# Optimization experiments

Measured on AMD Instinct MI355X. Metric: run time of the kernel, lower is better.

## Reference

```python
import jax, jax.numpy as jnp
import numpy as np

T, B, H = 512, 64, 1024

def setup_inputs() -> dict:
    key = jax.random.key(0)
    ks = jax.random.split(key, 16)
    names_mat = ['W_ir', 'W_hr', 'W_iz', 'W_hz', 'W_in', 'W_hn']
    names_vec = ['b_ir', 'b_hr', 'b_iz', 'b_hz', 'b_in', 'b_hn']
    inp = {
        'input_': jax.random.normal(ks[0], (T, B, H), dtype=jnp.float32),
        'hidden0': jax.random.normal(ks[1], (B, H), dtype=jnp.float32),
    }
    for i, n in enumerate(names_mat):
        inp[n] = jax.random.normal(ks[2 + i], (H, H), dtype=jnp.float32)
    for i, n in enumerate(names_vec):
        inp[n] = jax.random.normal(ks[8 + i], (H,), dtype=jnp.float32)
    # W = randn(H) * T, b = randn(1) in the original forward; made explicit here
    inp['W_out'] = jax.random.normal(ks[14], (H,), dtype=jnp.float32) * T
    inp['b_out'] = jax.random.normal(ks[15], (1,), dtype=jnp.float32)
    return inp

def reference(input_, hidden0, W_ir, W_hr, W_iz, W_hz, W_in, W_hn,
              b_ir, b_hr, b_iz, b_hz, b_in, b_hn, W_out, b_out):
    h = input_.shape[2]
    # permutation matrix is identity -> lower = tril(ones)
    lower = jnp.tril(jnp.ones((h, h), dtype=input_.dtype))
    Wir, Whr = W_ir * lower, W_hr * lower
    Wiz, Whz = W_iz * lower, W_hz * lower
    Win, Whn = W_in * lower, W_hn * lower

    def step(hid, x):
        # mask == x in the original call: cell(x, lower, x, hidden)
        r = jax.nn.sigmoid(x @ Wir + b_ir * x + hid @ Whr + b_hr)
        z = jax.nn.sigmoid(x @ Wiz + b_iz * x + hid @ Whz + b_hz)
        n = jnp.tanh(x @ Win + b_in * x + r * (hid @ Whn + b_hn))
        hid_new = hid * z + (1.0 - z) * n
        label = jax.nn.sigmoid(hid_new * W_out + b_out) * x  # [B, H]
        return hid_new, label

    _, labels = jax.lax.scan(step, hidden0, input_)  # labels: [T, B, H]
    ans_f = jnp.max(labels, axis=-1)                 # [T, B]
    ans = jnp.where(ans_f >= 0.5, 1, -1).astype(jnp.int32)
    return ans
```

## Files before the change

kernel.cpp:

```cpp
#include <hip/hip_runtime.h>

#define T_DIM 512
#define B_DIM 64
#define H_DIM 1024
#define NBLK 32
#define RING 64
#define AHEAD 62
#define KSLOT 33
#define APITCH 1032
#define FSTR 1024

typedef __attribute__((ext_vector_type(8))) short bf16x8;
typedef __attribute__((ext_vector_type(4))) float f32x4;


__device__ __forceinline__ unsigned short f2bf(float f) {
    unsigned u = __float_as_uint(f);
    unsigned r = (u + 0x7FFFu + ((u >> 16) & 1u)) >> 16;
    return (unsigned short)r;
}
__device__ __forceinline__ unsigned pack2(float a, float b) {
    return (unsigned)f2bf(a) | ((unsigned)f2bf(b) << 16);
}

__global__ __launch_bounds__(128) void prep_pack(
    const float* __restrict__ Wir, const float* __restrict__ Wiz, const float* __restrict__ Win,
    const float* __restrict__ Whr, const float* __restrict__ Whz, const float* __restrict__ Whn,
    unsigned short* __restrict__ Wpk)
{
    const float* srcs[6] = {Wir, Wiz, Win, Whr, Whz, Whn};
    const int bid   = blockIdx.x;
    const int g     = blockIdx.y;
    const int jt    = bid >> 6;
    const int jtile = (bid >> 5) & 1;
    const int ksrel = bid & 31;
    if (ksrel >= NBLK - jt) return;
    const int t    = threadIdx.x;
    const int lane = t >> 1, e0 = (t & 1) * 4;
    const float* src = srcs[g];
    const int j  = 32 * jt + 16 * jtile + (lane & 15);
    const int kb = (jt + ksrel) * 32 + (lane >> 4) * 8 + e0;
    ushort4 o; unsigned short* po = (unsigned short*)&o;
    #pragma unroll
    for (int i = 0; i < 4; ++i) {
        const int k = kb + i;
        const float w = (k >= j) ? src[(size_t)k * H_DIM + j] : 0.0f;
        po[i] = f2bf(w);
    }
    const size_t idx = ((((size_t)(jt * 2 + jtile) * KSLOT + ksrel) * 6 + g) * 64 + lane) * 8 + e0;
    *(ushort4*)(Wpk + idx) = o;
}

__global__ __launch_bounds__(256) void init_h(const float* __restrict__ h0,
                                              unsigned short* __restrict__ hring,
                                              unsigned* __restrict__ prog)
{
    if (blockIdx.x < 256) {
        const int i = blockIdx.x * 256 + threadIdx.x;
        hring[i] = f2bf(h0[i]);
    } else {
        unsigned* p = prog + (size_t)(blockIdx.x - 256) * 8192 + threadIdx.x;
        #pragma unroll
        for (int k = 0; k < 32; ++k) p[k * 256] = 0u;
    }
}

__global__ __launch_bounds__(512) void gru_main(
    const float* __restrict__ x,
    const unsigned short* __restrict__ Wpk,
    const float* __restrict__ bir, const float* __restrict__ bhr,
    const float* __restrict__ biz, const float* __restrict__ bhz,
    const float* __restrict__ bin_, const float* __restrict__ bhn,
    const float* __restrict__ Wout, const float* __restrict__ bout,
    const float* __restrict__ h0,
    unsigned short* __restrict__ hring,
    float* __restrict__ pmax,
    unsigned* __restrict__ prog)
{
    __shared__ __align__(16) unsigned short axf[8 * APITCH];
    __shared__ __align__(16) unsigned short ahf[8 * APITCH];
    __shared__ __align__(16) unsigned short zblk[8];
    __shared__ float red[8][6][64][4];
    __shared__ float hown[8][33];
    __shared__ unsigned short hb[8][32];

    const int tid  = threadIdx.x;
    const int lane = tid & 63;
    const int wv   = tid >> 6;

    const int jt = blockIdx.x & 31;
    const int bg = blockIdx.x >> 5;
    const int b0 = bg * 8;

    const int kcol0 = 32 * jt;
    const int CHN   = (H_DIM - kcol0) >> 3;
    const int cnt   = NBLK - jt;
    const int jtile = wv >> 2;
    const int ws4   = wv & 3;
    const int kpw   = (cnt + 3) >> 2;
    const int ks_s  = jt + ws4 * kpw;
    const int ks_e  = (ks_s + kpw < NBLK) ? (ks_s + kpw) : NBLK;

    const int row = lane & 15;
    const int kg  = lane >> 4;
    const unsigned short* pax = (row < 8) ? &axf[row * APITCH + kg * 8] : zblk;
    const unsigned short* pah = (row < 8) ? &ahf[row * APITCH + kg * 8] : zblk;
    const int astride = (row < 8) ? 32 : 0;
    const unsigned short* pw0 = Wpk + (size_t)(jt * 2 + jtile) * KSLOT * 3072 + lane * 8;

    const int ecol = tid & 31;
    const int eb   = tid >> 5;
    const int ej   = 32 * jt + ecol;
    float c_bir = 0, c_bhr = 0, c_biz = 0, c_bhz = 0, c_bin = 0, c_bhn = 0, c_wo = 0, bo = 0;
    if (tid < 256) {
        c_bir = bir[ej]; c_bhr = bhr[ej]; c_biz = biz[ej]; c_bhz = bhz[ej];
        c_bin = bin_[ej]; c_bhn = bhn[ej]; c_wo = Wout[ej]; bo = bout[0];
    }

    unsigned* myflag = prog + (size_t)((bg << 5) + jt) * FSTR;
    unsigned* pollp  = prog + (size_t)((bg << 5) + (lane & 31)) * FSTR;
    unsigned* bpflag = prog + (size_t)(bg << 5) * FSTR;

    if (tid < 8) zblk[tid] = 0;
    if (tid < 256) hown[eb][ecol] = h0[(size_t)(b0 + eb) * H_DIM + ej];
    {
        const float* src = x + (size_t)(b0 + wv) * H_DIM + kcol0;
        #pragma unroll
        for (int s = 0; s < 2; ++s) {
            const int c8 = lane + (s << 6);
            if (c8 < CHN) {
                const float4 v0 = *(const float4*)(src + c8 * 8);
                const float4 v1 = *(const float4*)(src + c8 * 8 + 4);
                uint4 o = make_uint4(pack2(v0.x, v0.y), pack2(v0.z, v0.w),
                                     pack2(v1.x, v1.y), pack2(v1.z, v1.w));
                *(uint4*)&axf[wv * APITCH + c8 * 8] = o;
            }
        }
    }

    unsigned cachedf  = 0;
    unsigned cachedbp = 0;

    for (int t = 0; t < T_DIM; ++t) {
        const int slot_r = t & (RING - 1), slot_w = (t + 1) & (RING - 1);

        if (wv == 0) {
            const int kt = lane & 31;
            const int thr = (kt > jt) ? t : -0x40000000;
            if (!__all((int)cachedf >= thr)) {
                for (;;) {
                    cachedf = __hip_atomic_load(pollp, __ATOMIC_RELAXED,
                                                __HIP_MEMORY_SCOPE_AGENT);
                    if (__all((int)cachedf >= thr)) break;
                    __builtin_amdgcn_s_sleep(4);
                }
            }
            if (jt > 0 && (int)cachedbp < t - 31) {
                for (;;) {
                    cachedbp = __hip_atomic_load(bpflag, __ATOMIC_RELAXED,
                                                 __HIP_MEMORY_SCOPE_AGENT);
                    if ((int)cachedbp >= t - 31) break;
                    __builtin_amdgcn_s_sleep(16);
                }
            }
        }
        __syncthreads();

        {
            const unsigned short* base = hring +
                ((size_t)slot_r * B_DIM + b0 + wv) * H_DIM + kcol0;
            const int cA = lane, cB = lane + 64;
            const bool gA = (cA < CHN), gB = (cB < CHN);
            uint4 o0, o1;
            const unsigned short* a0 = base + cA * 8;
            const unsigned short* a1 = base + cB * 8;
            if (gA) asm volatile("global_load_dwordx4 %0, %1, off sc0 sc1" : "=v"(o0) : "v"(a0));
            if (gB) asm volatile("global_load_dwordx4 %0, %1, off sc0 sc1" : "=v"(o1) : "v"(a1));
            asm volatile("s_waitcnt vmcnt(0)" ::: "memory");
            if (gA) *(uint4*)&ahf[wv * APITCH + cA * 8] = o0;
            if (gB) *(uint4*)&ahf[wv * APITCH + cB * 8] = o1;
        }
        __syncthreads();

        f32x4 a0 = 0.f, a1 = 0.f, a2 = 0.f, a3 = 0.f, a4 = 0.f, a5 = 0.f;
        for (int ks = ks_s; ks < ks_e; ++ks) {
            const int off = (ks - jt) * astride;
            const bf16x8 ax = *(const bf16x8*)(pax + off);
            const bf16x8 ah = *(const bf16x8*)(pah + off);
            const unsigned short* pw = pw0 + (size_t)(ks - jt) * 3072;
            const bf16x8 w0 = *(const bf16x8*)(pw);
            const bf16x8 w1 = *(const bf16x8*)(pw + 512);
            const bf16x8 w2 = *(const bf16x8*)(pw + 1024);
            const bf16x8 w3 = *(const bf16x8*)(pw + 1536);
            const bf16x8 w4 = *(const bf16x8*)(pw + 2048);
            const bf16x8 w5 = *(const bf16x8*)(pw + 2560);
            a0 = __builtin_amdgcn_mfma_f32_16x16x32_bf16(ax, w0, a0, 0, 0, 0);
            a1 = __builtin_amdgcn_mfma_f32_16x16x32_bf16(ax, w1, a1, 0, 0, 0);
            a2 = __builtin_amdgcn_mfma_f32_16x16x32_bf16(ax, w2, a2, 0, 0, 0);
            a3 = __builtin_amdgcn_mfma_f32_16x16x32_bf16(ah, w3, a3, 0, 0, 0);
            a4 = __builtin_amdgcn_mfma_f32_16x16x32_bf16(ah, w4, a4, 0, 0, 0);
            a5 = __builtin_amdgcn_mfma_f32_16x16x32_bf16(ah, w5, a5, 0, 0, 0);
        }
        *(f32x4*)&red[wv][0][lane][0] = a0;
        *(f32x4*)&red[wv][1][lane][0] = a1;
        *(f32x4*)&red[wv][2][lane][0] = a2;
        *(f32x4*)&red[wv][3][lane][0] = a3;
        *(f32x4*)&red[wv][4][lane][0] = a4;
        *(f32x4*)&red[wv][5][lane][0] = a5;
        __syncthreads();

        if (tid < 256) {
            const int wb = (ecol >> 4) * 4;
            const int lp = ((eb >> 2) << 4) | (ecol & 15);
            const int rg = eb & 3;
            float s0 = 0, s1 = 0, s2 = 0, s3 = 0, s4 = 0, s5 = 0;
            #pragma unroll
            for (int w2i = 0; w2i < 4; ++w2i) {
                s0 += red[wb + w2i][0][lp][rg]; s1 += red[wb + w2i][1][lp][rg];
                s2 += red[wb + w2i][2][lp][rg]; s3 += red[wb + w2i][3][lp][rg];
                s4 += red[wb + w2i][4][lp][rg]; s5 += red[wb + w2i][5][lp][rg];
            }
            const float xv = x[(size_t)t * B_DIM * H_DIM + (size_t)(b0 + eb) * H_DIM + ej];
            const float hv = hown[eb][ecol];
            const float rp = s0 + c_bir * xv + c_bhr + s3;
            const float zp = s1 + c_biz * xv + c_bhz + s4;
            const float r  = 1.0f / (1.0f + expf(-rp));
            const float z  = 1.0f / (1.0f + expf(-zp));
            const float np = s2 + c_bin * xv + r * (s5 + c_bhn);
            const float n  = tanhf(np);
            const float hnew = hv * z + (1.0f - z) * n;
            hown[eb][ecol] = hnew;
            hb[eb][ecol] = f2bf(hnew);
            float lab = (1.0f / (1.0f + expf(-(hnew * c_wo + bo)))) * xv;
            #pragma unroll
            for (int off = 16; off; off >>= 1)
                lab = fmaxf(lab, __shfl_xor(lab, off));
            if (ecol == 0) pmax[((size_t)t * B_DIM + b0 + eb) * 32 + jt] = lab;
        }
        __syncthreads();

        if (tid < 128) {
            const int b = tid >> 4, cq = tid & 15;
            const unsigned val = (unsigned)hb[b][2 * cq] | ((unsigned)hb[b][2 * cq + 1] << 16);
            unsigned* dst = (unsigned*)(hring +
                ((size_t)slot_w * B_DIM + b0 + b) * H_DIM + 32 * jt) + cq;
            __hip_atomic_store(dst, val, __ATOMIC_RELAXED, __HIP_MEMORY_SCOPE_AGENT);
        }
        __syncthreads();
        if (tid == 0)
            __hip_atomic_store(myflag, (unsigned)(t + 1),
                               __ATOMIC_RELEASE, __HIP_MEMORY_SCOPE_AGENT);

        if (t < T_DIM - 1) {
            const float* src = x + (size_t)(t + 1) * B_DIM * H_DIM
                             + (size_t)(b0 + wv) * H_DIM + kcol0;
            #pragma unroll
            for (int s = 0; s < 2; ++s) {
                const int c8 = lane + (s << 6);
                if (c8 < CHN) {
                    const float4 v0 = *(const float4*)(src + c8 * 8);
                    const float4 v1 = *(const float4*)(src + c8 * 8 + 4);
                    uint4 o = make_uint4(pack2(v0.x, v0.y), pack2(v0.z, v0.w),
                                         pack2(v1.x, v1.y), pack2(v1.z, v1.w));
                    *(uint4*)&axf[wv * APITCH + c8 * 8] = o;
                }
            }
        }
    }
}

__global__ __launch_bounds__(256) void finalize(const float* __restrict__ pmax, int* __restrict__ out)
{
    const int i = blockIdx.x * 256 + threadIdx.x;
    if (i >= T_DIM * B_DIM) return;
    const float4* pm = (const float4*)(pmax + (size_t)i * 32);
    float m = -3.4e38f;
    #pragma unroll
    for (int q = 0; q < 8; ++q) {
        const float4 v = pm[q];
        m = fmaxf(m, fmaxf(fmaxf(v.x, v.y), fmaxf(v.z, v.w)));
    }
    out[i] = (m >= 0.5f) ? 1 : -1;
}

extern "C" void kernel_launch(void* const* d_in, const int* in_sizes, int n_in,
                              void* d_out, int out_size, void* d_ws, size_t ws_size,
                              hipStream_t stream)
{
    const float* x    = (const float*)d_in[0];
    const float* h0   = (const float*)d_in[1];
    const float* W_ir = (const float*)d_in[2];
    const float* W_hr = (const float*)d_in[3];
    const float* W_iz = (const float*)d_in[4];
    const float* W_hz = (const float*)d_in[5];
    const float* W_in = (const float*)d_in[6];
    const float* W_hn = (const float*)d_in[7];
    const float* b_ir = (const float*)d_in[8];
    const float* b_hr = (const float*)d_in[9];
    const float* b_iz = (const float*)d_in[10];
    const float* b_hz = (const float*)d_in[11];
    const float* b_in = (const float*)d_in[12];
    const float* b_hn = (const float*)d_in[13];
    const float* W_out = (const float*)d_in[14];
    const float* b_out = (const float*)d_in[15];

    unsigned short* Wpk   = (unsigned short*)d_ws;
    unsigned short* hring = Wpk + (size_t)NBLK * 2 * KSLOT * 3072;
    float* pmax = (float*)(hring + (size_t)RING * B_DIM * H_DIM);
    unsigned* prog = (unsigned*)(pmax + (size_t)T_DIM * B_DIM * 32);

    prep_pack<<<dim3(NBLK * 64, 6), 128, 0, stream>>>(W_ir, W_iz, W_in, W_hr, W_hz, W_hn, Wpk);
    init_h<<<dim3(288), 256, 0, stream>>>(h0, hring, prog);

    void* args[] = {(void*)&x, (void*)&Wpk,
                    (void*)&b_ir, (void*)&b_hr, (void*)&b_iz, (void*)&b_hz,
                    (void*)&b_in, (void*)&b_hn, (void*)&W_out, (void*)&b_out,
                    (void*)&h0, (void*)&hring, (void*)&pmax, (void*)&prog};
    hipError_t rc = hipLaunchCooperativeKernel((const void*)gru_main, dim3(256), dim3(512),
                                               args, 0, stream);
    (void)rc;

    finalize<<<dim3(T_DIM * B_DIM / 256), 256, 0, stream>>>(pmax, (int*)d_out);
}
```

Baseline: 5.665 ms.

## Load hidden state straight into registers and trim per-step barriers

```diff
diff --git a/kernel.cpp b/kernel.cpp
--- a/kernel.cpp
+++ b/kernel.cpp
@@ -4,15 +4,13 @@
 #define B_DIM 64
 #define H_DIM 1024
 #define NBLK 32
-#define RING 64
-#define AHEAD 62
+#define RING 128
 #define KSLOT 33
 #define APITCH 1032
 #define FSTR 1024
 
 typedef __attribute__((ext_vector_type(8))) short bf16x8;
 typedef __attribute__((ext_vector_type(4))) float f32x4;
-
 
 __device__ __forceinline__ unsigned short f2bf(float f) {
     unsigned u = __float_as_uint(f);
@@ -78,11 +76,8 @@
     unsigned* __restrict__ prog)
 {
     __shared__ __align__(16) unsigned short axf[8 * APITCH];
-    __shared__ __align__(16) unsigned short ahf[8 * APITCH];
     __shared__ __align__(16) unsigned short zblk[8];
     __shared__ float red[8][6][64][4];
-    __shared__ float hown[8][33];
-    __shared__ unsigned short hb[8][32];
 
     const int tid  = threadIdx.x;
     const int lane = tid & 63;
@@ -100,11 +95,12 @@
     const int kpw   = (cnt + 3) >> 2;
     const int ks_s  = jt + ws4 * kpw;
     const int ks_e  = (ks_s + kpw < NBLK) ? (ks_s + kpw) : NBLK;
+    const int nsl   = (ks_e > ks_s) ? (ks_e - ks_s) : 0;
 
     const int row = lane & 15;
     const int kg  = lane >> 4;
+    const int hrow = (row < 8) ? row : 0;
     const unsigned short* pax = (row < 8) ? &axf[row * APITCH + kg * 8] : zblk;
-    const unsigned short* pah = (row < 8) ? &ahf[row * APITCH + kg * 8] : zblk;
     const int astride = (row < 8) ? 32 : 0;
     const unsigned short* pw0 = Wpk + (size_t)(jt * 2 + jtile) * KSLOT * 3072 + lane * 8;
 
@@ -112,9 +108,11 @@
     const int eb   = tid >> 5;
     const int ej   = 32 * jt + ecol;
     float c_bir = 0, c_bhr = 0, c_biz = 0, c_bhz = 0, c_bin = 0, c_bhn = 0, c_wo = 0, bo = 0;
+    float hreg = 0.0f;
     if (tid < 256) {
         c_bir = bir[ej]; c_bhr = bhr[ej]; c_biz = biz[ej]; c_bhz = bhz[ej];
         c_bin = bin_[ej]; c_bhn = bhn[ej]; c_wo = Wout[ej]; bo = bout[0];
+        hreg = h0[(size_t)(b0 + eb) * H_DIM + ej];
     }
 
     unsigned* myflag = prog + (size_t)((bg << 5) + jt) * FSTR;
@@ -122,7 +120,6 @@
     unsigned* bpflag = prog + (size_t)(bg << 5) * FSTR;
 
     if (tid < 8) zblk[tid] = 0;
-    if (tid < 256) hown[eb][ecol] = h0[(size_t)(b0 + eb) * H_DIM + ej];
     {
         const float* src = x + (size_t)(b0 + wv) * H_DIM + kcol0;
         #pragma unroll
@@ -148,58 +145,62 @@
             const int kt = lane & 31;
             const int thr = (kt > jt) ? t : -0x40000000;
             if (!__all((int)cachedf >= thr)) {
+                int spins = 0;
                 for (;;) {
                     cachedf = __hip_atomic_load(pollp, __ATOMIC_RELAXED,
                                                 __HIP_MEMORY_SCOPE_AGENT);
                     if (__all((int)cachedf >= thr)) break;
-                    __builtin_amdgcn_s_sleep(4);
+                    if (++spins > 24) __builtin_amdgcn_s_sleep(4);
                 }
             }
-            if (jt > 0 && (int)cachedbp < t - 31) {
+            if (jt > 0 && (int)cachedbp < t - 95) {
                 for (;;) {
                     cachedbp = __hip_atomic_load(bpflag, __ATOMIC_RELAXED,
                                                  __HIP_MEMORY_SCOPE_AGENT);
-                    if ((int)cachedbp >= t - 31) break;
-                    __builtin_amdgcn_s_sleep(16);
+                    if ((int)cachedbp >= t - 95) break;
+                    __builtin_amdgcn_s_sleep(8);
                 }
             }
         }
         __syncthreads();
 
+        uint4 hf[8];
         {
-            const unsigned short* base = hring +
-                ((size_t)slot_r * B_DIM + b0 + wv) * H_DIM + kcol0;
-            const int cA = lane, cB = lane + 64;
-            const bool gA = (cA < CHN), gB = (cB < CHN);
-            uint4 o0, o1;
-            const unsigned short* a0 = base + cA * 8;
-            const unsigned short* a1 = base + cB * 8;
-            if (gA) asm volatile("global_load_dwordx4 %0, %1, off sc0 sc1" : "=v"(o0) : "v"(a0));
-            if (gB) asm volatile("global_load_dwordx4 %0, %1, off sc0 sc1" : "=v"(o1) : "v"(a1));
+            const unsigned short* hbase = hring +
+                ((size_t)slot_r * B_DIM + b0 + hrow) * H_DIM;
+            #pragma unroll
+            for (int s = 0; s < 8; ++s) {
+                hf[s] = make_uint4(0u, 0u, 0u, 0u);
+                if (s < nsl && row < 8) {
+                    const unsigned short* a = hbase + (ks_s + s) * 32 + kg * 8;
+                    asm volatile("global_load_dwordx4 %0, %1, off sc0 sc1"
+                                 : "=v"(hf[s]) : "v"(a));
+                }
+            }
             asm volatile("s_waitcnt vmcnt(0)" ::: "memory");
-            if (gA) *(uint4*)&ahf[wv * APITCH + cA * 8] = o0;
-            if (gB) *(uint4*)&ahf[wv * APITCH + cB * 8] = o1;
-        }
-        __syncthreads();
+        }
 
         f32x4 a0 = 0.f, a1 = 0.f, a2 = 0.f, a3 = 0.f, a4 = 0.f, a5 = 0.f;
-        for (int ks = ks_s; ks < ks_e; ++ks) {
-            const int off = (ks - jt) * astride;
-            const bf16x8 ax = *(const bf16x8*)(pax + off);
-            const bf16x8 ah = *(const bf16x8*)(pah + off);
-            const unsigned short* pw = pw0 + (size_t)(ks - jt) * 3072;
-            const bf16x8 w0 = *(const bf16x8*)(pw);
-            const bf16x8 w1 = *(const bf16x8*)(pw + 512);
-            const bf16x8 w2 = *(const bf16x8*)(pw + 1024);
-            const bf16x8 w3 = *(const bf16x8*)(pw + 1536);
-            const bf16x8 w4 = *(const bf16x8*)(pw + 2048);
-            const bf16x8 w5 = *(const bf16x8*)(pw + 2560);
-            a0 = __builtin_amdgcn_mfma_f32_16x16x32_bf16(ax, w0, a0, 0, 0, 0);
-            a1 = __builtin_amdgcn_mfma_f32_16x16x32_bf16(ax, w1, a1, 0, 0, 0);
-            a2 = __builtin_amdgcn_mfma_f32_16x16x32_bf16(ax, w2, a2, 0, 0, 0);
-            a3 = __builtin_amdgcn_mfma_f32_16x16x32_bf16(ah, w3, a3, 0, 0, 0);
-            a4 = __builtin_amdgcn_mfma_f32_16x16x32_bf16(ah, w4, a4, 0, 0, 0);
-            a5 = __builtin_amdgcn_mfma_f32_16x16x32_bf16(ah, w5, a5, 0, 0, 0);
+        #pragma unroll
+        for (int s = 0; s < 8; ++s) {
+            if (s < nsl) {
+                const int ks = ks_s + s;
+                const bf16x8 ax = *(const bf16x8*)(pax + (ks - jt) * astride);
+                const bf16x8 ah = *(const bf16x8*)&hf[s];
+                const unsigned short* pw = pw0 + (size_t)(ks - jt) * 3072;
+                const bf16x8 w0 = *(const bf16x8*)(pw);
+                const bf16x8 w1 = *(const bf16x8*)(pw + 512);
+                const bf16x8 w2 = *(const bf16x8*)(pw + 1024);
+                const bf16x8 w3 = *(const bf16x8*)(pw + 1536);
+                const bf16x8 w4 = *(const bf16x8*)(pw + 2048);
+                const bf16x8 w5 = *(const bf16x8*)(pw + 2560);
+                a0 = __builtin_amdgcn_mfma_f32_16x16x32_bf16(ax, w0, a0, 0, 0, 0);
+                a1 = __builtin_amdgcn_mfma_f32_16x16x32_bf16(ax, w1, a1, 0, 0, 0);
+                a2 = __builtin_amdgcn_mfma_f32_16x16x32_bf16(ax, w2, a2, 0, 0, 0);
+                a3 = __builtin_amdgcn_mfma_f32_16x16x32_bf16(ah, w3, a3, 0, 0, 0);
+                a4 = __builtin_amdgcn_mfma_f32_16x16x32_bf16(ah, w4, a4, 0, 0, 0);
+                a5 = __builtin_amdgcn_mfma_f32_16x16x32_bf16(ah, w5, a5, 0, 0, 0);
+            }
         }
         *(f32x4*)&red[wv][0][lane][0] = a0;
         *(f32x4*)&red[wv][1][lane][0] = a1;
@@ -221,51 +222,51 @@
                 s4 += red[wb + w2i][4][lp][rg]; s5 += red[wb + w2i][5][lp][rg];
             }
             const float xv = x[(size_t)t * B_DIM * H_DIM + (size_t)(b0 + eb) * H_DIM + ej];
-            const float hv = hown[eb][ecol];
             const float rp = s0 + c_bir * xv + c_bhr + s3;
             const float zp = s1 + c_biz * xv + c_bhz + s4;
             const float r  = 1.0f / (1.0f + expf(-rp));
             const float z  = 1.0f / (1.0f + expf(-zp));
             const float np = s2 + c_bin * xv + r * (s5 + c_bhn);
             const float n  = tanhf(np);
-            const float hnew = hv * z + (1.0f - z) * n;
-            hown[eb][ecol] = hnew;
-            hb[eb][ecol] = f2bf(hnew);
+            const float hnew = hreg * z + (1.0f - z) * n;
+            hreg = hnew;
+            const unsigned mybf = (unsigned)f2bf(hnew);
+            const unsigned other = (unsigned)__shfl_xor((int)mybf, 1);
+            if ((ecol & 1) == 0) {
+                const unsigned val = mybf | (other << 16);
+                unsigned* dst = (unsigned*)(hring +
+                    ((size_t)slot_w * B_DIM + b0 + eb) * H_DIM + 32 * jt + ecol);
+                __hip_atomic_store(dst, val, __ATOMIC_RELAXED, __HIP_MEMORY_SCOPE_AGENT);
+            }
             float lab = (1.0f / (1.0f + expf(-(hnew * c_wo + bo)))) * xv;
             #pragma unroll
             for (int off = 16; off; off >>= 1)
                 lab = fmaxf(lab, __shfl_xor(lab, off));
             if (ecol == 0) pmax[((size_t)t * B_DIM + b0 + eb) * 32 + jt] = lab;
+        } else if (t < T_DIM - 1) {
+            const float* xs = x + (size_t)(t + 1) * B_DIM * H_DIM;
+            #pragma unroll
+            for (int rr = 0; rr < 2; ++rr) {
+                const int r = 2 * (wv - 4) + rr;
+                const float* src = xs + (size_t)(b0 + r) * H_DIM + kcol0;
+                #pragma unroll
+                for (int s = 0; s < 2; ++s) {
+                    const int c8 = lane + (s << 6);
+                    if (c8 < CHN) {
+                        const float4 v0 = *(const float4*)(src + c8 * 8);
+                        const float4 v1 = *(const float4*)(src + c8 * 8 + 4);
+                        uint4 o = make_uint4(pack2(v0.x, v0.y), pack2(v0.z, v0.w),
+                                             pack2(v1.x, v1.y), pack2(v1.z, v1.w));
+                        *(uint4*)&axf[r * APITCH + c8 * 8] = o;
+                    }
+                }
+            }
         }
         __syncthreads();
 
-        if (tid < 128) {
-            const int b = tid >> 4, cq = tid & 15;
-            const unsigned val = (unsigned)hb[b][2 * cq] | ((unsigned)hb[b][2 * cq + 1] << 16);
-            unsigned* dst = (unsigned*)(hring +
-                ((size_t)slot_w * B_DIM + b0 + b) * H_DIM + 32 * jt) + cq;
-            __hip_atomic_store(dst, val, __ATOMIC_RELAXED, __HIP_MEMORY_SCOPE_AGENT);
-        }
-        __syncthreads();
         if (tid == 0)
             __hip_atomic_store(myflag, (unsigned)(t + 1),
                                __ATOMIC_RELEASE, __HIP_MEMORY_SCOPE_AGENT);
-
-        if (t < T_DIM - 1) {
-            const float* src = x + (size_t)(t + 1) * B_DIM * H_DIM
-                             + (size_t)(b0 + wv) * H_DIM + kcol0;
-            #pragma unroll
-            for (int s = 0; s < 2; ++s) {
-                const int c8 = lane + (s << 6);
-                if (c8 < CHN) {
-                    const float4 v0 = *(const float4*)(src + c8 * 8);
-                    const float4 v1 = *(const float4*)(src + c8 * 8 + 4);
-                    uint4 o = make_uint4(pack2(v0.x, v0.y), pack2(v0.z, v0.w),
-                                         pack2(v1.x, v1.y), pack2(v1.z, v1.w));
-                    *(uint4*)&axf[wv * APITCH + c8 * 8] = o;
-                }
-            }
-        }
     }
 }
 
```

Measured after the change: 6.157 ms. 8.7% more time.

## Split recurrent matmul into far and near K-chunks to overlap dependency waits

Applied to the files above, without the earlier changes.

```diff
diff --git a/kernel.cpp b/kernel.cpp
--- a/kernel.cpp
+++ b/kernel.cpp
@@ -5,14 +5,12 @@
 #define H_DIM 1024
 #define NBLK 32
 #define RING 64
-#define AHEAD 62
 #define KSLOT 33
 #define APITCH 1032
 #define FSTR 1024
 
 typedef __attribute__((ext_vector_type(8))) short bf16x8;
 typedef __attribute__((ext_vector_type(4))) float f32x4;
-
 
 __device__ __forceinline__ unsigned short f2bf(float f) {
     unsigned u = __float_as_uint(f);
@@ -81,8 +79,6 @@
     __shared__ __align__(16) unsigned short ahf[8 * APITCH];
     __shared__ __align__(16) unsigned short zblk[8];
     __shared__ float red[8][6][64][4];
-    __shared__ float hown[8][33];
-    __shared__ unsigned short hb[8][32];
 
     const int tid  = threadIdx.x;
     const int lane = tid & 63;
@@ -101,6 +97,11 @@
     const int ks_s  = jt + ws4 * kpw;
     const int ks_e  = (ks_s + kpw < NBLK) ? (ks_s + kpw) : NBLK;
 
+    const int kb     = (jt + 2 < NBLK) ? (jt + 2) : NBLK;
+    const int nearch = 4 * (kb - jt);
+    const int fs     = (ks_s > kb) ? ks_s : kb;
+    const int ne     = (ks_e < kb) ? ks_e : kb;
+
     const int row = lane & 15;
     const int kg  = lane >> 4;
     const unsigned short* pax = (row < 8) ? &axf[row * APITCH + kg * 8] : zblk;
@@ -112,9 +113,11 @@
     const int eb   = tid >> 5;
     const int ej   = 32 * jt + ecol;
     float c_bir = 0, c_bhr = 0, c_biz = 0, c_bhz = 0, c_bin = 0, c_bhn = 0, c_wo = 0, bo = 0;
+    float hreg = 0.0f;
     if (tid < 256) {
         c_bir = bir[ej]; c_bhr = bhr[ej]; c_biz = biz[ej]; c_bhz = bhz[ej];
         c_bin = bin_[ej]; c_bhn = bhn[ej]; c_wo = Wout[ej]; bo = bout[0];
+        hreg = h0[(size_t)(b0 + eb) * H_DIM + ej];
     }
 
     unsigned* myflag = prog + (size_t)((bg << 5) + jt) * FSTR;
@@ -122,7 +125,6 @@
     unsigned* bpflag = prog + (size_t)(bg << 5) * FSTR;
 
     if (tid < 8) zblk[tid] = 0;
-    if (tid < 256) hown[eb][ecol] = h0[(size_t)(b0 + eb) * H_DIM + ej];
     {
         const float* src = x + (size_t)(b0 + wv) * H_DIM + kcol0;
         #pragma unroll
@@ -146,13 +148,14 @@
 
         if (wv == 0) {
             const int kt = lane & 31;
-            const int thr = (kt > jt) ? t : -0x40000000;
-            if (!__all((int)cachedf >= thr)) {
+            const int thrF = (kt >= kb) ? t : -0x40000000;
+            if (!__all((int)cachedf >= thrF)) {
+                int spins = 0;
                 for (;;) {
                     cachedf = __hip_atomic_load(pollp, __ATOMIC_RELAXED,
                                                 __HIP_MEMORY_SCOPE_AGENT);
-                    if (__all((int)cachedf >= thr)) break;
-                    __builtin_amdgcn_s_sleep(4);
+                    if (__all((int)cachedf >= thrF)) break;
+                    if (++spins > 24) __builtin_amdgcn_s_sleep(4);
                 }
             }
             if (jt > 0 && (int)cachedbp < t - 31) {
@@ -170,7 +173,7 @@
             const unsigned short* base = hring +
                 ((size_t)slot_r * B_DIM + b0 + wv) * H_DIM + kcol0;
             const int cA = lane, cB = lane + 64;
-            const bool gA = (cA < CHN), gB = (cB < CHN);
+            const bool gA = (cA >= nearch && cA < CHN), gB = (cB >= nearch && cB < CHN);
             uint4 o0, o1;
             const unsigned short* a0 = base + cA * 8;
             const unsigned short* a1 = base + cB * 8;
@@ -183,7 +186,7 @@
         __syncthreads();
 
         f32x4 a0 = 0.f, a1 = 0.f, a2 = 0.f, a3 = 0.f, a4 = 0.f, a5 = 0.f;
-        for (int ks = ks_s; ks < ks_e; ++ks) {
+        for (int ks = fs; ks < ks_e; ++ks) {
             const int off = (ks - jt) * astride;
             const bf16x8 ax = *(const bf16x8*)(pax + off);
             const bf16x8 ah = *(const bf16x8*)(pah + off);
@@ -201,6 +204,52 @@
             a4 = __builtin_amdgcn_mfma_f32_16x16x32_bf16(ah, w4, a4, 0, 0, 0);
             a5 = __builtin_amdgcn_mfma_f32_16x16x32_bf16(ah, w5, a5, 0, 0, 0);
         }
+
+        if (wv == 0) {
+            const int kt = lane & 31;
+            const int thrN = (kt > jt && kt < kb) ? t : -0x40000000;
+            if (!__all((int)cachedf >= thrN)) {
+                int spins = 0;
+                for (;;) {
+                    cachedf = __hip_atomic_load(pollp, __ATOMIC_RELAXED,
+                                                __HIP_MEMORY_SCOPE_AGENT);
+                    if (__all((int)cachedf >= thrN)) break;
+                    if (++spins > 64) __builtin_amdgcn_s_sleep(2);
+                }
+            }
+        }
+        __syncthreads();
+
+        {
+            const unsigned short* base = hring +
+                ((size_t)slot_r * B_DIM + b0 + wv) * H_DIM + kcol0;
+            uint4 o0;
+            const bool gA = (lane < nearch);
+            const unsigned short* a0p = base + lane * 8;
+            if (gA) asm volatile("global_load_dwordx4 %0, %1, off sc0 sc1" : "=v"(o0) : "v"(a0p));
+            asm volatile("s_waitcnt vmcnt(0)" ::: "memory");
+            if (gA) *(uint4*)&ahf[wv * APITCH + lane * 8] = o0;
+        }
+        __syncthreads();
+
+        for (int ks = ks_s; ks < ne; ++ks) {
+            const int off = (ks - jt) * astride;
+            const bf16x8 ax = *(const bf16x8*)(pax + off);
+            const bf16x8 ah = *(const bf16x8*)(pah + off);
+            const unsigned short* pw = pw0 + (size_t)(ks - jt) * 3072;
+            const bf16x8 w0 = *(const bf16x8*)(pw);
+            const bf16x8 w1 = *(const bf16x8*)(pw + 512);
+            const bf16x8 w2 = *(const bf16x8*)(pw + 1024);
+            const bf16x8 w3 = *(const bf16x8*)(pw + 1536);
+            const bf16x8 w4 = *(const bf16x8*)(pw + 2048);
+            const bf16x8 w5 = *(const bf16x8*)(pw + 2560);
+            a0 = __builtin_amdgcn_mfma_f32_16x16x32_bf16(ax, w0, a0, 0, 0, 0);
+            a1 = __builtin_amdgcn_mfma_f32_16x16x32_bf16(ax, w1, a1, 0, 0, 0);
+            a2 = __builtin_amdgcn_mfma_f32_16x16x32_bf16(ax, w2, a2, 0, 0, 0);
+            a3 = __builtin_amdgcn_mfma_f32_16x16x32_bf16(ah, w3, a3, 0, 0, 0);
+            a4 = __builtin_amdgcn_mfma_f32_16x16x32_bf16(ah, w4, a4, 0, 0, 0);
+            a5 = __builtin_amdgcn_mfma_f32_16x16x32_bf16(ah, w5, a5, 0, 0, 0);
+        }
         *(f32x4*)&red[wv][0][lane][0] = a0;
         *(f32x4*)&red[wv][1][lane][0] = a1;
         *(f32x4*)&red[wv][2][lane][0] = a2;
@@ -209,6 +258,7 @@
         *(f32x4*)&red[wv][5][lane][0] = a5;
         __syncthreads();
 
+        float xv = 0.0f;
         if (tid < 256) {
             const int wb = (ecol >> 4) * 4;
             const int lp = ((eb >> 2) << 4) | (ecol & 15);
@@ -220,51 +270,54 @@
                 s2 += red[wb + w2i][2][lp][rg]; s3 += red[wb + w2i][3][lp][rg];
                 s4 += red[wb + w2i][4][lp][rg]; s5 += red[wb + w2i][5][lp][rg];
             }
-            const float xv = x[(size_t)t * B_DIM * H_DIM + (size_t)(b0 + eb) * H_DIM + ej];
-            const float hv = hown[eb][ecol];
+            xv = x[(size_t)t * B_DIM * H_DIM + (size_t)(b0 + eb) * H_DIM + ej];
             const float rp = s0 + c_bir * xv + c_bhr + s3;
             const float zp = s1 + c_biz * xv + c_bhz + s4;
             const float r  = 1.0f / (1.0f + expf(-rp));
             const float z  = 1.0f / (1.0f + expf(-zp));
             const float np = s2 + c_bin * xv + r * (s5 + c_bhn);
             const float n  = tanhf(np);
-            const float hnew = hv * z + (1.0f - z) * n;
-            hown[eb][ecol] = hnew;
-            hb[eb][ecol] = f2bf(hnew);
-            float lab = (1.0f / (1.0f + expf(-(hnew * c_wo + bo)))) * xv;
+            const float hnew = hreg * z + (1.0f - z) * n;
+            hreg = hnew;
+            const unsigned mybf = (unsigned)f2bf(hnew);
+            const unsigned other = (unsigned)__shfl_xor((int)mybf, 1);
+            if ((ecol & 1) == 0) {
+                const unsigned val = mybf | (other << 16);
+                unsigned* dst = (unsigned*)(hring +
+                    ((size_t)slot_w * B_DIM + b0 + eb) * H_DIM + 32 * jt + ecol);
+                __hip_atomic_store(dst, val, __ATOMIC_RELAXED, __HIP_MEMORY_SCOPE_AGENT);
+            }
+        } else if (t < T_DIM - 1) {
+            const float* xs = x + (size_t)(t + 1) * B_DIM * H_DIM;
+            #pragma unroll
+            for (int rr = 0; rr < 2; ++rr) {
+                const int r = 2 * (wv - 4) + rr;
+                const float* src = xs + (size_t)(b0 + r) * H_DIM + kcol0;
+                #pragma unroll
+                for (int s = 0; s < 2; ++s) {
+                    const int c8 = lane + (s << 6);
+                    if (c8 < CHN) {
+                        const float4 v0 = *(const float4*)(src + c8 * 8);
+                        const float4 v1 = *(const float4*)(src + c8 * 8 + 4);
+                        uint4 o = make_uint4(pack2(v0.x, v0.y), pack2(v0.z, v0.w),
+                                             pack2(v1.x, v1.y), pack2(v1.z, v1.w));
+                        *(uint4*)&axf[r * APITCH + c8 * 8] = o;
+                    }
+                }
+            }
+        }
+        __syncthreads();
+
+        if (tid == 0)
+            __hip_atomic_store(myflag, (unsigned)(t + 1),
+                               __ATOMIC_RELEASE, __HIP_MEMORY_SCOPE_AGENT);
+
+        if (tid < 256) {
+            float lab = (1.0f / (1.0f + expf(-(hreg * c_wo + bo)))) * xv;
             #pragma unroll
             for (int off = 16; off; off >>= 1)
                 lab = fmaxf(lab, __shfl_xor(lab, off));
             if (ecol == 0) pmax[((size_t)t * B_DIM + b0 + eb) * 32 + jt] = lab;
-        }
-        __syncthreads();
-
-        if (tid < 128) {
-            const int b = tid >> 4, cq = tid & 15;
-            const unsigned val = (unsigned)hb[b][2 * cq] | ((unsigned)hb[b][2 * cq + 1] << 16);
-            unsigned* dst = (unsigned*)(hring +
-                ((size_t)slot_w * B_DIM + b0 + b) * H_DIM + 32 * jt) + cq;
-            __hip_atomic_store(dst, val, __ATOMIC_RELAXED, __HIP_MEMORY_SCOPE_AGENT);
-        }
-        __syncthreads();
-        if (tid == 0)
-            __hip_atomic_store(myflag, (unsigned)(t + 1),
-                               __ATOMIC_RELEASE, __HIP_MEMORY_SCOPE_AGENT);
-
-        if (t < T_DIM - 1) {
-            const float* src = x + (size_t)(t + 1) * B_DIM * H_DIM
-                             + (size_t)(b0 + wv) * H_DIM + kcol0;
-            #pragma unroll
-            for (int s = 0; s < 2; ++s) {
-                const int c8 = lane + (s << 6);
-                if (c8 < CHN) {
-                    const float4 v0 = *(const float4*)(src + c8 * 8);
-                    const float4 v1 = *(const float4*)(src + c8 * 8 + 4);
-                    uint4 o = make_uint4(pack2(v0.x, v0.y), pack2(v0.z, v0.w),
-                                         pack2(v1.x, v1.y), pack2(v1.z, v1.w));
-                    *(uint4*)&axf[wv * APITCH + c8 * 8] = o;
-                }
-            }
         }
     }
 }
```

New measurement: 6.037 ms. 1.07x slower.
